# Kernel optimization log

Measured on AMD Instinct MI355X. Metric: run time of the kernel, lower is better.

Reference implementation:

```python
import jax, jax.numpy as jnp
import numpy as np

VOCAB, D, N, K, L = 6144, 1024, 4, 8, 3
D_FF, N_STREAMS, SINK_ITERS = 3072, 4, 20
ALPHA = 4.0      # surrogate sigmoid sharpness
EK_FLOOR = 0.0
B, S = 4, 128

@jax.custom_vjp
def spike(x):
    return (x >= 0.).astype(x.dtype)

def _spike_fwd(x):
    return (x >= 0.).astype(x.dtype), x

def _spike_bwd(x, g):
    s = jax.nn.sigmoid(ALPHA * x)
    return (g * ALPHA * s * (1. - s),)

spike.defvjp(_spike_fwd, _spike_bwd)

def plif_scan(beta, x, v_th):
    # PLIF recurrence over leading time axis. x: (T,B,C); beta, v_th: (C,).
    # v_t = beta*v + (1-beta)*x_t ; heaviside spike (sigmoid surrogate); soft reset.
    # Returns spike current v_th * spike (matches spike_current_activation).
    def step(v, x_t):
        v = beta * v + (1. - beta) * x_t
        s = spike(v - v_th)
        return v - v_th * s, v_th * s
    v0 = jnp.zeros(x.shape[1:], x.dtype)
    _, cur = jax.lax.scan(step, v0, x)
    return cur

def sinkhorn(logits):
    # doubly-stochastic projection (Birkhoff polytope), fixed iteration count
    M = jnp.exp(logits)
    for _ in range(SINK_ITERS):
        M = M / M.sum(1, keepdims=True)
        M = M / M.sum(0, keepdims=True)
    return M

def rmsnorm(x, w, eps=1e-6):
    return x * w * jax.lax.rsqrt(jnp.mean(x * x, axis=-1, keepdims=True) + eps)

def lateral_inhibition(x, w, eps=1e-6):
    xc = x - x.mean(axis=-1, keepdims=True)
    return w * xc * jax.lax.rsqrt(jnp.mean(xc * xc, axis=-1, keepdims=True) + eps)

LAYER_KEYS = ['H_logits','w_pre','w_post','beta_in1','vth_in1','W_in','beta_h','vth_h','W_out','beta_in2','vth_in2','W_gate','beta_gate','vth_gate','W_up','beta_up','vth_up','W_down','halt_w','halt_b']

def layer_forward(h, p):
    # h: (S, B, n, D) multi-stream residual
    Sq, Bq = h.shape[0], h.shape[1]
    H = sinkhorn(p['H_logits'])                                   # (n,n) doubly stochastic
    h_mix = jnp.einsum('mn,sbnd->sbmd', H, h)                     # mHC stream mixing
    x = jnp.einsum('n,sbnd->sbd', jax.nn.softmax(p['w_pre']), h_mix)
    x_tk = jnp.repeat(x, K, axis=0)                               # (S*K, B, D) K-frame unroll
    s1 = plif_scan(p['beta_in1'], x_tk, p['vth_in1'])             # input_neuron1
    sh = plif_scan(p['beta_h'], s1 @ p['W_in'], p['vth_h'])       # snn_block hidden (N*D)
    y_blk = sh @ p['W_out']                                       # (TK,B,D)
    s2 = plif_scan(p['beta_in2'], x_tk + y_blk, p['vth_in2'])     # input_neuron2
    g = plif_scan(p['beta_gate'], s2 @ p['W_gate'], p['vth_gate'])  # snn_ffn gate
    u = plif_scan(p['beta_up'], s2 @ p['W_up'], p['vth_up'])        # snn_ffn up
    y = y_blk + (g * u) @ p['W_down']                             # (TK,B,D)
    yk = y.reshape(Sq, K, Bq, D)
    # PonderNet halting over the K frames of each token
    lam = jax.nn.sigmoid(jnp.einsum('skbd,d->skb', yk, p['halt_w']) + p['halt_b'])
    keep = jnp.cumprod(1. - lam, axis=1)
    prev = jnp.concatenate([jnp.ones_like(keep[:, :1]), keep[:, :-1]], axis=1)
    pk = lam * prev
    pk = pk.at[:, -1].add(1. - pk.sum(axis=1))                    # remainder to last frame
    y_tok = jnp.einsum('skb,skbd->sbd', pk, yk)
    ek = jnp.einsum('skb,k->sb', pk, jnp.arange(1, K + 1, dtype=y.dtype)).mean()
    efc = jnp.maximum(EK_FLOOR - ek, 0.)
    w_post = jax.nn.softmax(p['w_post'])
    h_out = h_mix + w_post[None, None, :, None] * y_tok[:, :, None, :]
    return h_out, ek, efc

def _forward(token_ids, embed, norm_w, decode_W, decode_b, out_norm_w, beta_out, vth_out, stacked):
    emb = embed[token_ids]                                        # (B,S,D)
    h = jnp.transpose(emb, (1, 0, 2))[:, :, None, :]
    h = jnp.broadcast_to(h, (emb.shape[1], emb.shape[0], N_STREAMS, D))  # (S,B,n,D)
    pcs, efcs = [], []
    for l in range(L):
        p = {k: stacked[k][l] for k in LAYER_KEYS}
        h, pc, efc = layer_forward(h, p)
        pcs.append(pc); efcs.append(efc)
    ponder = sum(pcs) / L
    ekf = sum(efcs) / L
    # decode: collapse streams -> K-frame output neuron -> tied embedding logits
    h_coll = h.mean(axis=2)                                       # (S,B,D)
    h_tk = jnp.repeat(h_coll, K, axis=0)                          # (S*K,B,D)
    h_tk = rmsnorm(h_tk, out_norm_w)
    cur = plif_scan(beta_out, h_tk, vth_out)
    decoded = cur.reshape(h_coll.shape[0], K, h_coll.shape[1], D).mean(axis=1)
    decoded = jnp.transpose(decoded, (1, 0, 2))                   # (B,S,D)
    hh = decoded @ decode_W.T + decode_b
    hh = lateral_inhibition(hh, norm_w)
    logits = hh @ embed.T                                         # tied embedding
    return logits, ponder, ekf

def setup_inputs() -> dict:
    key = jax.random.key(0)
    ks = iter(jax.random.split(key, 48))
    def nrm(shape, std):
        return jax.random.normal(next(ks), shape, jnp.float32) * std
    def beta_init(shape):
        return 0.4 + 0.4 * jax.random.uniform(next(ks), shape, jnp.float32)
    def vth_init(shape):
        return 0.1 + 0.3 * jax.random.uniform(next(ks), shape, jnp.float32)
    inp = dict(
        token_ids=jax.random.randint(next(ks), (B, S), 0, VOCAB),
        embed=nrm((VOCAB, D), 0.02),
        norm_w=jnp.ones((D,), jnp.float32),
        decode_W=nrm((D, D), 1. / np.sqrt(D)),
        decode_b=jnp.zeros((D,), jnp.float32),
        out_norm_w=jnp.ones((D,), jnp.float32),
        beta_out=beta_init((D,)), vth_out=vth_init((D,)),
        H_logits=nrm((L, N_STREAMS, N_STREAMS), 0.1),
        w_pre=nrm((L, N_STREAMS), 0.1),
        w_post=nrm((L, N_STREAMS), 0.1),
        beta_in1=beta_init((L, D)), vth_in1=vth_init((L, D)),
        W_in=nrm((L, D, N * D), 1. / np.sqrt(D)),
        beta_h=beta_init((L, N * D)), vth_h=vth_init((L, N * D)),
        W_out=nrm((L, N * D, D), 1. / np.sqrt(N * D)),
        beta_in2=beta_init((L, D)), vth_in2=vth_init((L, D)),
        W_gate=nrm((L, D, D_FF), 1. / np.sqrt(D)),
        beta_gate=beta_init((L, D_FF)), vth_gate=vth_init((L, D_FF)),
        W_up=nrm((L, D, D_FF), 1. / np.sqrt(D)),
        beta_up=beta_init((L, D_FF)), vth_up=vth_init((L, D_FF)),
        W_down=nrm((L, D_FF, D), 1. / np.sqrt(D_FF)),
        halt_w=nrm((L, D), 0.02),
        halt_b=jnp.full((L,), 1.0, jnp.float32),
    )
    return inp

def reference(token_ids, embed, norm_w, decode_W, decode_b, out_norm_w, beta_out, vth_out, H_logits, w_pre, w_post, beta_in1, vth_in1, W_in, beta_h, vth_h, W_out, beta_in2, vth_in2, W_gate, beta_gate, vth_gate, W_up, beta_up, vth_up, W_down, halt_w, halt_b):
    stacked = dict(H_logits=H_logits, w_pre=w_pre, w_post=w_post, beta_in1=beta_in1, vth_in1=vth_in1, W_in=W_in, beta_h=beta_h, vth_h=vth_h, W_out=W_out, beta_in2=beta_in2, vth_in2=vth_in2, W_gate=W_gate, beta_gate=beta_gate, vth_gate=vth_gate, W_up=W_up, beta_up=beta_up, vth_up=vth_up, W_down=W_down, halt_w=halt_w, halt_b=halt_b)
    return _forward(token_ids, embed, norm_w, decode_W, decode_b, out_norm_w, beta_out, vth_out, stacked)
```

## Files before the change

### kernel.cpp

```cpp
#include <hip/hip_runtime.h>
#include <hip/hip_bf16.h>

#define B 4
#define S 128
#define D 1024
#define NS 4
#define KF 8
#define LNUM 3
#define DFF 3072
#define ND 4096
#define T 1024
#define TB 4096
#define VOCABSZ 6144
#define SINKIT 20

typedef unsigned short u16;
typedef __attribute__((ext_vector_type(8))) short short8;
typedef __attribute__((ext_vector_type(4))) float f32x4;

__device__ __forceinline__ void gload16(const void* g, void* l) {
  __builtin_amdgcn_global_load_lds(
      (const __attribute__((address_space(1))) void*)g,
      (__attribute__((address_space(3))) void*)l, 16, 0, 0);
}

__global__ void sink_kernel(const float* __restrict__ Hl, const float* __restrict__ wpre,
                            const float* __restrict__ wpost, float* __restrict__ prm) {
  if (threadIdx.x != 0 || blockIdx.x != 0) return;
  float M[16];
  for (int i = 0; i < 16; ++i) M[i] = expf(Hl[i]);
  for (int it = 0; it < SINKIT; ++it) {
    for (int m = 0; m < 4; ++m) {
      float s = M[m*4+0] + M[m*4+1] + M[m*4+2] + M[m*4+3];
      for (int n = 0; n < 4; ++n) M[m*4+n] /= s;
    }
    for (int n = 0; n < 4; ++n) {
      float s = M[0*4+n] + M[1*4+n] + M[2*4+n] + M[3*4+n];
      for (int m = 0; m < 4; ++m) M[m*4+n] /= s;
    }
  }
  for (int i = 0; i < 16; ++i) prm[i] = M[i];
  float a[4], mx, sm;
  mx = fmaxf(fmaxf(wpre[0], wpre[1]), fmaxf(wpre[2], wpre[3]));
  sm = 0.f; for (int i = 0; i < 4; ++i) { a[i] = expf(wpre[i] - mx); sm += a[i]; }
  for (int i = 0; i < 4; ++i) prm[16+i] = a[i] / sm;
  mx = fmaxf(fmaxf(wpost[0], wpost[1]), fmaxf(wpost[2], wpost[3]));
  sm = 0.f; for (int i = 0; i < 4; ++i) { a[i] = expf(wpost[i] - mx); sm += a[i]; }
  for (int i = 0; i < 4; ++i) prm[20+i] = a[i] / sm;
}

__global__ __launch_bounds__(256)
void gather_kernel(const int* __restrict__ tok, const float* __restrict__ embed,
                   float* __restrict__ h) {
  const int idx = blockIdx.x * 256 + threadIdx.x;
  const int d   = idx % D;
  const int sbn = idx / D;
  const int sb  = sbn / NS;
  const int b   = sb % B, s = sb / B;
  h[idx] = embed[(size_t)tok[b*S + s] * D + d];
}

__global__ __launch_bounds__(256)
void mix_kernel(const float* __restrict__ h, const float* __restrict__ P,
                float* __restrict__ h_mix, float* __restrict__ x) {
  const int idx = blockIdx.x * 256 + threadIdx.x;
  const int d = idx % D, sb = idx / D;
  const float* hp = h + (size_t)sb * NS * D + d;
  const float h0 = hp[0], h1 = hp[D], h2 = hp[2*D], h3 = hp[3*D];
  float xv = 0.f;
  #pragma unroll
  for (int m = 0; m < 4; ++m) {
    float hm = P[m*4+0]*h0 + P[m*4+1]*h1 + P[m*4+2]*h2 + P[m*4+3]*h3;
    h_mix[(size_t)sb * NS * D + m*D + d] = hm;
    xv = fmaf(P[16+m], hm, xv);
  }
  x[idx] = xv;
}

template<bool R1, bool A2>
__global__ __launch_bounds__(256)
void plif_kernel(const float* __restrict__ z1, const float* __restrict__ z2,
                 const float* __restrict__ beta, const float* __restrict__ vth,
                 u16* __restrict__ outp, int C) {
  const int idx = blockIdx.x * 256 + threadIdx.x;
  const int c = idx % C;
  const int stride = B * C;
  const float be = beta[c], vt = vth[c], omb = 1.f - be;
  float v = 0.f;
  constexpr int PF = 32;
  float xA[PF], yA[PF], xB[PF], yB[PF];

#define PLOAD(xa, ya, tb) do {                                               \
    if (R1) {                                                                \
      _Pragma("unroll")                                                      \
      for (int i = 0; i < PF/8; ++i)                                         \
        xa[i] = z1[(size_t)((tb)/8 + i) * stride + idx];                     \
    } else {                                                                 \
      _Pragma("unroll")                                                      \
      for (int i = 0; i < PF; ++i)                                           \
        xa[i] = z1[(size_t)((tb) + i) * stride + idx];                       \
    }                                                                        \
    if (A2) {                                                                \
      _Pragma("unroll")                                                      \
      for (int i = 0; i < PF; ++i)                                           \
        ya[i] = z2[(size_t)((tb) + i) * stride + idx];                       \
    }                                                                        \
  } while (0)

#define PCOMP(xa, ya, tb) do {                                               \
    _Pragma("unroll")                                                        \
    for (int i = 0; i < PF; ++i) {                                           \
      float xt = R1 ? xa[i >> 3] : xa[i];                                    \
      if (A2) xt += ya[i];                                                   \
      v = fmaf(be, v, omb * xt);                                             \
      const bool sp = (v >= vt);                                             \
      if (sp) v -= vt;                                                       \
      outp[(size_t)((tb) + i) * stride + idx] = sp ? (u16)0x3F80 : (u16)0;   \
    }                                                                        \
  } while (0)

  PLOAD(xA, yA, 0);
  for (int tb = 0; tb < T; tb += 2*PF) {
    PLOAD(xB, yB, tb + PF);
    PCOMP(xA, yA, tb);
    if (tb + 2*PF < T) PLOAD(xA, yA, tb + 2*PF);
    PCOMP(xB, yB, tb + PF);
  }
#undef PLOAD
#undef PCOMP
}

__global__ __launch_bounds__(256)
void plif_gu_kernel(const float* __restrict__ z12,
                    const float* __restrict__ bg, const float* __restrict__ vg_,
                    const float* __restrict__ bu, const float* __restrict__ vu_,
                    u16* __restrict__ outp) {
  const int idx = blockIdx.x * 256 + threadIdx.x;
  const int c = idx % DFF, b = idx / DFF;
  const float beg = bg[c], vtg = vg_[c], beu = bu[c], vtu = vu_[c];
  const float og = 1.f - beg, ou = 1.f - beu;
  float vg = 0.f, vu = 0.f;
  constexpr int PF = 32;
  float gA[PF], uA[PF], gB[PF], uB[PF];

#define GLOAD_(ga, ua, tb) do {                                              \
    _Pragma("unroll")                                                        \
    for (int i = 0; i < PF; ++i) {                                           \
      const size_t off_ = ((size_t)((tb) + i) * B + b) * (2*DFF) + c;        \
      ga[i] = z12[off_];                                                     \
      ua[i] = z12[off_ + DFF];                                               \
    }                                                                        \
  } while (0)

#define GCOMP_(ga, ua, tb) do {                                              \
    _Pragma("unroll")                                                        \
    for (int i = 0; i < PF; ++i) {                                           \
      vg = fmaf(beg, vg, og * ga[i]);                                        \
      vu = fmaf(beu, vu, ou * ua[i]);                                        \
      const bool sg = (vg >= vtg), su = (vu >= vtu);                         \
      if (sg) vg -= vtg;                                                     \
      if (su) vu -= vtu;                                                     \
      outp[(size_t)((tb) + i) * (B*DFF) + idx] = (sg && su) ? (u16)0x3F80 : (u16)0; \
    }                                                                        \
  } while (0)

  GLOAD_(gA, uA, 0);
  for (int tb = 0; tb < T; tb += 2*PF) {
    GLOAD_(gB, uB, tb + PF);
    GCOMP_(gA, uA, tb);
    if (tb + 2*PF < T) GLOAD_(gA, uA, tb + 2*PF);
    GCOMP_(gB, uB, tb + PF);
  }
#undef GLOAD_
#undef GCOMP_
}

__global__ __launch_bounds__(256)
void prep_t_kernel(const float* __restrict__ W, const float* __restrict__ sA,
                   const float* __restrict__ sB, float mult,
                   u16* __restrict__ wt, int Kd, int Nd) {
  __shared__ float tile[64][65];
  const int tid = threadIdx.x;
  const int bn = blockIdx.x, bk = blockIdx.y;
  const int c = tid & 63, r0 = (tid >> 6) * 16;
  #pragma unroll
  for (int i = 0; i < 16; ++i) {
    const int r = r0 + i;
    const int kg = bk*64 + r;
    float s = mult;
    if (sA) s *= sA[kg];
    if (sB) s *= sB[kg];
    tile[r][c] = W[(size_t)kg * Nd + bn*64 + c] * s;
  }
  __syncthreads();
  const int K2 = 2 * Kd;
  #pragma unroll
  for (int i = 0; i < 16; ++i) {
    const int nl = r0 + i;
    const float v = tile[c][nl];
    const __hip_bfloat16 h = __float2bfloat16(v);
    const size_t off = (size_t)(bn*64 + nl) * K2 + bk*64 + c;
    wt[off] = *(const u16*)&h;
    const __hip_bfloat16 lo = __float2bfloat16(v - __bfloat162float(h));
    wt[off + Kd] = *(const u16*)&lo;
  }
}

__global__ __launch_bounds__(256)
void prep_nt_kernel(const float* __restrict__ W, const float* __restrict__ sK, float mult,
                    u16* __restrict__ wt, int Kd) {
  const size_t idx = (size_t)blockIdx.x * 256 + threadIdx.x;
  const int k = (int)(idx % Kd);
  const size_t n = idx / Kd;
  const float v = W[idx] * mult * (sK ? sK[k] : 1.f);
  const __hip_bfloat16 h = __float2bfloat16(v);
  const size_t off = n * (2*Kd) + k;
  wt[off] = *(const u16*)&h;
  const __hip_bfloat16 lo = __float2bfloat16(v - __bfloat162float(h));
  wt[off + Kd] = *(const u16*)&lo;
}


template<bool ADDC>
__global__ __launch_bounds__(256)
void mgemm2_kernel(const u16* __restrict__ A, const u16* __restrict__ Bm,
                   const float* __restrict__ Cin, float* __restrict__ Cout,
                   int M, int N, int Astride, int AW, int BW, int Bstride, int K2) {
  __shared__ __align__(16) char lds[49152];
  const int tid = threadIdx.x;
  const int lane = tid & 63, wv = tid >> 6;
  const int wm = wv >> 1, wn = wv & 1;
  const int lr = lane & 15, ks = lane >> 4;
  const int rs3 = (lr >> 1) & 3;

  const int gx = gridDim.x;
  const int nwg = gx * gridDim.y;
  int flat = blockIdx.y * gx + blockIdx.x;
  flat = (flat & 7) * (nwg >> 3) + (flat >> 3);
  const int bn = flat % gx, bm = flat / gx;

  f32x4 acc[4][4];
  #pragma unroll
  for (int i = 0; i < 4; ++i)
    #pragma unroll
    for (int j = 0; j < 4; ++j) acc[i][j] = (f32x4){0.f, 0.f, 0.f, 0.f};

  const size_t am0 = (size_t)bm * 128, bn0 = (size_t)bn * 128;

#define STAGE(bufbase, k0) do {                                                  \
    const int aoff_ = ((k0) >= AW) ? (k0) - AW : (k0);                           \
    const int boff_ = ((k0) >= BW) ? (k0) - BW : (k0);                           \
    _Pragma("unroll")                                                            \
    for (int c_ = 0; c_ < 2; ++c_) {                                             \
      const int bo_ = c_*4096 + wv*1024 + lane*16;                               \
      const int row_ = bo_ >> 6;                                                 \
      const int csrc_ = ((bo_ >> 4) & 3) ^ ((row_ >> 1) & 3);                    \
      gload16((const char*)A + ((am0 + row_) * (size_t)Astride + aoff_ + csrc_*8) * 2, \
              lds + (bufbase) + c_*4096 + wv*1024);                              \
      gload16((const char*)Bm + ((bn0 + row_) * (size_t)Bstride + boff_ + csrc_*8) * 2, \
              lds + (bufbase) + 8192 + c_*4096 + wv*1024);                       \
    }                                                                            \
  } while (0)

  const int nt = K2 >> 5;
  STAGE(0, 0);
  if (nt > 1) STAGE(16384, 32);
  int bc = 0;
  for (int t = 0; t < nt; ++t) {
    if (t + 2 < nt) {
      int bs = bc + 2; if (bs >= 3) bs -= 3;
      STAGE(bs * 16384, (t + 2) << 5);
      asm volatile("s_waitcnt vmcnt(8)\n\ts_barrier" ::: "memory");
    } else if (t + 1 < nt) {
      asm volatile("s_waitcnt vmcnt(4)\n\ts_barrier" ::: "memory");
    } else {
      asm volatile("s_waitcnt vmcnt(0)\n\ts_barrier" ::: "memory");
    }
    const char* la = lds + bc * 16384;
    const char* lb = la + 8192;
    short8 af[4], bf[4];
    #pragma unroll
    for (int f = 0; f < 4; ++f) {
      af[f] = *(const short8*)(la + (wm*64 + f*16 + lr)*64 + ((ks ^ rs3) * 16));
      bf[f] = *(const short8*)(lb + (wn*64 + f*16 + lr)*64 + ((ks ^ rs3) * 16));
    }
    #pragma unroll
    for (int i = 0; i < 4; ++i)
      #pragma unroll
      for (int j = 0; j < 4; ++j)
        acc[i][j] = __builtin_amdgcn_mfma_f32_16x16x32_bf16(af[i], bf[j], acc[i][j], 0, 0, 0);
    asm volatile("s_barrier" ::: "memory");
    bc = bc + 1; if (bc >= 3) bc = 0;
  }
#undef STAGE

  const int col0 = bn*128 + wn*64 + lr;
  #pragma unroll
  for (int i = 0; i < 4; ++i)
    #pragma unroll
    for (int j = 0; j < 4; ++j) {
      const size_t rbase = (size_t)(bm*128 + wm*64 + i*16 + ks*4);
      #pragma unroll
      for (int r = 0; r < 4; ++r) {
        const size_t idx = (rbase + r) * (size_t)N + col0 + j*16;
        float v = acc[i][j][r];
        if (ADDC) v += Cin[idx];
        Cout[idx] = v;
      }
    }
}

__global__ __launch_bounds__(512)
void mgemm3_kernel(const u16* __restrict__ A, const u16* __restrict__ Bm,
                   float* __restrict__ Cout, int M, int N, int Astride, int AW, int K2) {
  __shared__ __align__(16) char lds[98304];
  const int tid = threadIdx.x;
  const int lane = tid & 63, wv = tid >> 6;
  const int wm = wv >> 2, wn = wv & 3;
  const int lr = lane & 15, ks = lane >> 4;
  const int rs3 = (lr >> 1) & 3;

  const int gx = gridDim.x;
  const int nwg = gx * gridDim.y;
  int flat = blockIdx.y * gx + blockIdx.x;
  flat = (flat & 7) * (nwg >> 3) + (flat >> 3);
  const int bn = flat % gx, bm = flat / gx;

  f32x4 acc[8][4];
  #pragma unroll
  for (int i = 0; i < 8; ++i)
    #pragma unroll
    for (int j = 0; j < 4; ++j) acc[i][j] = (f32x4){0.f, 0.f, 0.f, 0.f};

  const size_t am0 = (size_t)bm * 256, bn0 = (size_t)bn * 256;

#define STG(base, k0) do {                                                        \
    const int aoff_ = ((k0) >= AW) ? (k0) - AW : (k0);                            \
    _Pragma("unroll")                                                             \
    for (int c_ = 0; c_ < 2; ++c_) {                                              \
      const int fl_ = c_*8192 + wv*1024 + lane*16;                                \
      const int row_ = fl_ >> 6;                                                  \
      const int csrc_ = ((fl_ >> 4) & 3) ^ ((row_ >> 1) & 3);                     \
      gload16((const char*)A + ((am0 + row_) * (size_t)Astride + aoff_ + csrc_*8) * 2, \
              lds + (base) + c_*8192 + wv*1024);                                  \
      gload16((const char*)Bm + ((bn0 + row_) * (size_t)K2 + (k0) + csrc_*8) * 2, \
              lds + (base) + 16384 + c_*8192 + wv*1024);                          \
    }                                                                             \
  } while (0)

  const int nt = K2 >> 5;
  STG(0, 0);
  if (nt > 1) STG(32768, 32);
  int bc = 0;
  for (int t = 0; t < nt; ++t) {
    if (t + 2 < nt) {
      int bs = bc + 2; if (bs >= 3) bs -= 3;
      STG(bs * 32768, (t + 2) << 5);
      asm volatile("s_waitcnt vmcnt(8)\n\ts_barrier" ::: "memory");
    } else if (t + 1 < nt) {
      asm volatile("s_waitcnt vmcnt(4)\n\ts_barrier" ::: "memory");
    } else {
      asm volatile("s_waitcnt vmcnt(0)\n\ts_barrier" ::: "memory");
    }
    const char* la = lds + bc * 32768;
    const char* lb = la + 16384;
    short8 af[8], bf[4];
    #pragma unroll
    for (int i = 0; i < 8; ++i)
      af[i] = *(const short8*)(la + (wm*128 + i*16 + lr)*64 + ((ks ^ rs3) * 16));
    #pragma unroll
    for (int j = 0; j < 4; ++j)
      bf[j] = *(const short8*)(lb + (wn*64 + j*16 + lr)*64 + ((ks ^ rs3) * 16));
    __builtin_amdgcn_s_setprio(1);
    #pragma unroll
    for (int i = 0; i < 8; ++i)
      #pragma unroll
      for (int j = 0; j < 4; ++j)
        acc[i][j] = __builtin_amdgcn_mfma_f32_16x16x32_bf16(af[i], bf[j], acc[i][j], 0, 0, 0);
    __builtin_amdgcn_s_setprio(0);
    asm volatile("s_barrier" ::: "memory");
    bc = bc + 1; if (bc >= 3) bc = 0;
  }
#undef STG

  const int col0 = bn*256 + wn*64 + lr;
  #pragma unroll
  for (int i = 0; i < 8; ++i)
    #pragma unroll
    for (int j = 0; j < 4; ++j) {
      const size_t rbase = (size_t)(bm*256 + wm*128 + i*16 + ks*4);
      #pragma unroll
      for (int r = 0; r < 4; ++r)
        Cout[(rbase + r) * (size_t)N + col0 + j*16] = acc[i][j][r];
    }
}

__global__ __launch_bounds__(256)
void halt_kernel(const float* __restrict__ y, const float* __restrict__ h_mix,
                 const float* __restrict__ P, const float* __restrict__ hw,
                 const float* __restrict__ hb, float* __restrict__ h_out,
                 float* __restrict__ ek_acc) {
  const int sb = blockIdx.x;
  const int b = sb % B, s = sb / B;
  const int tid = threadIdx.x;
  __shared__ float red[256];
  __shared__ float lam_s[KF];
  __shared__ float pk_s[KF];

  for (int k = 0; k < KF; ++k) {
    const float* yr = y + ((size_t)(s*KF + k) * B + b) * D;
    float p = 0.f;
    for (int d = tid; d < D; d += 256) p = fmaf(yr[d], hw[d], p);
    red[tid] = p; __syncthreads();
    for (int off = 128; off > 0; off >>= 1) {
      if (tid < off) red[tid] += red[tid + off];
      __syncthreads();
    }
    if (tid == 0) lam_s[k] = 1.f / (1.f + expf(-(red[0] + hb[0])));
    __syncthreads();
  }
  if (tid == 0) {
    float keep = 1.f, sum = 0.f, pk[KF];
    #pragma unroll
    for (int k = 0; k < KF; ++k) { pk[k] = lam_s[k] * keep; keep *= (1.f - lam_s[k]); sum += pk[k]; }
    pk[KF-1] += 1.f - sum;
    float ek = 0.f;
    #pragma unroll
    for (int k = 0; k < KF; ++k) { ek += pk[k] * (float)(k + 1); pk_s[k] = pk[k]; }
    atomicAdd(ek_acc, ek);
  }
  __syncthreads();
  for (int d = tid; d < D; d += 256) {
    float yt = 0.f;
    #pragma unroll
    for (int k = 0; k < KF; ++k)
      yt = fmaf(pk_s[k], y[((size_t)(s*KF + k) * B + b) * D + d], yt);
    #pragma unroll
    for (int n = 0; n < NS; ++n) {
      const size_t off = ((size_t)sb * NS + n) * D + d;
      h_out[off] = h_mix[off] + P[20+n] * yt;
    }
  }
}

__global__ __launch_bounds__(256)
void collnorm_kernel(const float* __restrict__ h, const float* __restrict__ w,
                     float* __restrict__ xn) {
  const int sb = blockIdx.x, tid = threadIdx.x;
  __shared__ float red[256];
  float vals[4]; float ss = 0.f;
  #pragma unroll
  for (int i = 0; i < 4; ++i) {
    const int d = tid + i*256;
    const float* hp = h + (size_t)sb * NS * D + d;
    float m = 0.25f * (hp[0] + hp[D] + hp[2*D] + hp[3*D]);
    vals[i] = m; ss += m*m;
  }
  red[tid] = ss; __syncthreads();
  for (int off = 128; off > 0; off >>= 1) { if (tid < off) red[tid] += red[tid + off]; __syncthreads(); }
  const float inv = 1.f / sqrtf(red[0] * (1.f/(float)D) + 1e-6f);
  #pragma unroll
  for (int i = 0; i < 4; ++i) {
    const int d = tid + i*256;
    xn[(size_t)sb * D + d] = vals[i] * w[d] * inv;
  }
}

__global__ __launch_bounds__(256)
void dplif_kernel(const float* __restrict__ xn, const float* __restrict__ beta,
                  const float* __restrict__ vth, u16* __restrict__ dec) {
  const int idx = blockIdx.x * 256 + threadIdx.x;
  const int b = idx / D, d = idx % D;
  const float be = beta[d], vt = vth[d], omb = 1.f - be;
  float v = 0.f;
  for (int s = 0; s < S; ++s) {
    const float xv = xn[((size_t)s * B + b) * D + d];
    float cnt = 0.f;
    #pragma unroll
    for (int k = 0; k < KF; ++k) {
      v = fmaf(be, v, omb * xv);
      if (v >= vt) { v -= vt; cnt += 1.f; }
    }
    const __hip_bfloat16 hb_ = __float2bfloat16(cnt);
    dec[((size_t)b * S + s) * D + d] = *(const u16*)&hb_;
  }
}

__global__ __launch_bounds__(256)
void li_kernel(float* __restrict__ hh, const float* __restrict__ bias,
               const float* __restrict__ w) {
  const int r = blockIdx.x, tid = threadIdx.x;
  __shared__ float red[256];
  float* row = hh + (size_t)r * D;
  float v[4]; float sm = 0.f;
  #pragma unroll
  for (int i = 0; i < 4; ++i) { const int d = tid + i*256; v[i] = row[d] + bias[d]; sm += v[i]; }
  red[tid] = sm; __syncthreads();
  for (int off = 128; off > 0; off >>= 1) { if (tid < off) red[tid] += red[tid + off]; __syncthreads(); }
  const float mean = red[0] * (1.f/(float)D);
  __syncthreads();
  float ss = 0.f;
  #pragma unroll
  for (int i = 0; i < 4; ++i) { v[i] -= mean; ss += v[i]*v[i]; }
  red[tid] = ss; __syncthreads();
  for (int off = 128; off > 0; off >>= 1) { if (tid < off) red[tid] += red[tid + off]; __syncthreads(); }
  const float inv = 1.f / sqrtf(red[0] * (1.f/(float)D) + 1e-6f);
  #pragma unroll
  for (int i = 0; i < 4; ++i) { const int d = tid + i*256; row[d] = w[d] * v[i] * inv; }
}

__global__ __launch_bounds__(256)
void split_kernel(const float* __restrict__ X, u16* __restrict__ xs, int Kd) {
  const size_t idx = (size_t)blockIdx.x * 256 + threadIdx.x;
  const int k = (int)(idx % Kd);
  const size_t n = idx / Kd;
  const float v = X[idx];
  const __hip_bfloat16 h = __float2bfloat16(v);
  const size_t off = n * (2*Kd) + k;
  xs[off] = *(const u16*)&h;
  const __hip_bfloat16 lo = __float2bfloat16(v - __bfloat162float(h));
  xs[off + Kd] = *(const u16*)&lo;
}

__global__ void finalize_kernel(const float* __restrict__ ek_acc, float* __restrict__ tail) {
  if (threadIdx.x != 0 || blockIdx.x != 0) return;
  float ponder = 0.f, ekf = 0.f;
  for (int l = 0; l < LNUM; ++l) {
    float ek = ek_acc[l] * (1.f/(float)(S*B));
    ponder += ek;
    ekf += fmaxf(0.f - ek, 0.f);
  }
  tail[0] = ponder * (1.f/(float)LNUM);
  tail[1] = ekf * (1.f/(float)LNUM);
}

extern "C" void kernel_launch(void* const* d_in, const int* in_sizes, int n_in,
                              void* d_out, int out_size, void* d_ws, size_t ws_size,
                              hipStream_t stream) {
  const int*   tok       = (const int*)  d_in[0];
  const float* embed     = (const float*)d_in[1];
  const float* norm_w    = (const float*)d_in[2];
  const float* decode_W  = (const float*)d_in[3];
  const float* decode_b  = (const float*)d_in[4];
  const float* out_norm  = (const float*)d_in[5];
  const float* beta_out  = (const float*)d_in[6];
  const float* vth_out   = (const float*)d_in[7];
  const float* H_logits  = (const float*)d_in[8];
  const float* w_pre     = (const float*)d_in[9];
  const float* w_post    = (const float*)d_in[10];
  const float* beta_in1  = (const float*)d_in[11];
  const float* vth_in1   = (const float*)d_in[12];
  const float* W_in      = (const float*)d_in[13];
  const float* beta_h    = (const float*)d_in[14];
  const float* vth_h     = (const float*)d_in[15];
  const float* W_out     = (const float*)d_in[16];
  const float* beta_in2  = (const float*)d_in[17];
  const float* vth_in2   = (const float*)d_in[18];
  const float* W_gate    = (const float*)d_in[19];
  const float* beta_gate = (const float*)d_in[20];
  const float* vth_gate  = (const float*)d_in[21];
  const float* W_up      = (const float*)d_in[22];
  const float* beta_up   = (const float*)d_in[23];
  const float* vth_up    = (const float*)d_in[24];
  const float* W_down    = (const float*)d_in[25];
  const float* halt_w    = (const float*)d_in[26];
  const float* halt_b    = (const float*)d_in[27];
  float* out = (float*)d_out;

  float* ws = (float*)d_ws;
  size_t o = 0;
  float* prm   = ws + o; o += 256;
  float* h_cur = ws + o; o += (size_t)S*B*NS*D;
  float* h_mix = ws + o; o += (size_t)S*B*NS*D;
  float* xbuf  = ws + o; o += (size_t)S*B*D;
  float* y_blk = ws + o; o += (size_t)TB*D;
  float* zbig  = ws + o; o += (size_t)TB*2*DFF;
  u16*   spb   = (u16*)(ws + o); o += (size_t)TB*ND/2;
  u16*   s1b   = (u16*)(ws + o); o += (size_t)TB*D/2;
  u16*   s2b   = (u16*)(ws + o); o += (size_t)TB*D/2;
  float* xn    = ws + o; o += (size_t)S*B*D;
  u16*   decb  = (u16*)(ws + o); o += (size_t)B*S*D/2;
  float* hh    = ws + o; o += (size_t)B*S*D;
  u16*   wt    = (u16*)(ws + o); o += (size_t)(2*DFF)*D;
  if (ws_size < o * sizeof(float)) return;

  float* ek_acc = prm + 96;
  hipMemsetAsync(ek_acc, 0, 3 * sizeof(float), stream);

  gather_kernel<<<(S*B*NS*D)/256, 256, 0, stream>>>(tok, embed, h_cur);

  for (int l = 0; l < LNUM; ++l) {
    float* P = prm + l*32;
    sink_kernel<<<1, 64, 0, stream>>>(H_logits + l*16, w_pre + l*4, w_post + l*4, P);
    mix_kernel<<<(S*B*D)/256, 256, 0, stream>>>(h_cur, P, h_mix, xbuf);
    plif_kernel<true,false><<<(B*D)/256, 256, 0, stream>>>(
        xbuf, nullptr, beta_in1 + l*D, vth_in1 + l*D, s1b, D);

    { dim3 gp(ND/64, D/64);
      prep_t_kernel<<<gp, 256, 0, stream>>>(W_in + (size_t)l*D*ND, vth_in1 + l*D, nullptr, 1.f,
                                            wt, D, ND); }
    { dim3 g(ND/256, TB/256);
      mgemm3_kernel<<<g, 512, 0, stream>>>(s1b, wt, zbig, TB, ND, D, D, 2*D); }
    plif_kernel<false,false><<<(B*ND)/256, 256, 0, stream>>>(
        zbig, nullptr, beta_h + l*ND, vth_h + l*ND, spb, ND);

    { dim3 gp(D/64, ND/64);
      prep_t_kernel<<<gp, 256, 0, stream>>>(W_out + (size_t)l*ND*D, vth_h + l*ND, nullptr, 1.f,
                                            wt, ND, D); }
    { dim3 g(D/128, TB/128);
      mgemm2_kernel<false><<<g, 256, 0, stream>>>(spb, wt, nullptr, y_blk, TB, D,
                                                  ND, ND, 2*ND, 2*ND, 2*ND); }
    plif_kernel<true,true><<<(B*D)/256, 256, 0, stream>>>(
        xbuf, y_blk, beta_in2 + l*D, vth_in2 + l*D, s2b, D);

    { dim3 gp(DFF/64, D/64);
      prep_t_kernel<<<gp, 256, 0, stream>>>(W_gate + (size_t)l*D*DFF, vth_in2 + l*D, nullptr, 1.f,
                                            wt, D, DFF);
      prep_t_kernel<<<gp, 256, 0, stream>>>(W_up + (size_t)l*D*DFF, vth_in2 + l*D, nullptr, 1.f,
                                            wt + (size_t)DFF*2*D, D, DFF); }
    { dim3 g((2*DFF)/256, TB/256);
      mgemm3_kernel<<<g, 512, 0, stream>>>(s2b, wt, zbig, TB, 2*DFF, D, D, 2*D); }
    plif_gu_kernel<<<(B*DFF)/256, 256, 0, stream>>>(
        zbig, beta_gate + l*DFF, vth_gate + l*DFF, beta_up + l*DFF, vth_up + l*DFF, spb);

    { dim3 gp(D/64, DFF/64);
      prep_t_kernel<<<gp, 256, 0, stream>>>(W_down + (size_t)l*DFF*D, vth_gate + l*DFF,
                                            vth_up + l*DFF, 1.f, wt, DFF, D); }
    { dim3 g(D/128, TB/128);
      mgemm2_kernel<true><<<g, 256, 0, stream>>>(spb, wt, y_blk, y_blk, TB, D,
                                                 DFF, DFF, 2*DFF, 2*DFF, 2*DFF); }
    halt_kernel<<<S*B, 256, 0, stream>>>(y_blk, h_mix, P, halt_w + l*D, halt_b + l, h_cur, ek_acc + l);
  }

  collnorm_kernel<<<S*B, 256, 0, stream>>>(h_cur, out_norm, xn);
  dplif_kernel<<<(B*D)/256, 256, 0, stream>>>(xn, beta_out, vth_out, decb);

  prep_nt_kernel<<<(D*D)/256, 256, 0, stream>>>(decode_W, vth_out, 0.125f, wt, D);
  { dim3 g(D/128, (B*S)/128);
    mgemm2_kernel<false><<<g, 256, 0, stream>>>(decb, wt, nullptr, hh, B*S, D,
                                                D, D, 2*D, 2*D, 2*D); }
  li_kernel<<<B*S, 256, 0, stream>>>(hh, decode_b, norm_w);

  u16* hh_c  = (u16*)(zbig + 6600000);
  u16* emb_c = (u16*)zbig;
  split_kernel<<<(B*S*D)/256, 256, 0, stream>>>(hh, hh_c, D);
  prep_nt_kernel<<<(VOCABSZ*D)/256, 256, 0, stream>>>(embed, nullptr, 1.f, emb_c, D);
  { dim3 g(VOCABSZ/128, (B*S)/128);
    mgemm2_kernel<false><<<g, 256, 0, stream>>>(hh_c, emb_c, nullptr, out, B*S, VOCABSZ,
                                                2*D, D, 2*D, 2*D, 3*D); }
  finalize_kernel<<<1, 1, 0, stream>>>(ek_acc, out + (out_size - 2));
}
```

Baseline: 2.124 ms.

## Restructure 256x256 GEMM into 8-phase ping-pong pipeline with half-tile staging

Rewrites the mgemm3 main loop from a 3-stage, 32-wide K pipeline into a double-buffered, 64-wide K schedule. Each iteration is split into eight phases that each compute a quadrant of the output tile. Every phase interleaves the LDS fragment reads, the issue of one half-tile global-to-LDS load, and the MFMA block, with explicit vmcnt waits and barriers. The goal is finer-grained overlap of memory traffic with MFMA work, in the style of the hipBLASLt/HipKittens 8-wave ping-pong. In exchange it raises LDS use to 128KB, adds more barriers, and assumes K2 is a multiple of 128.

```diff
diff --git a/kernel.cpp b/kernel.cpp
--- a/kernel.cpp
+++ b/kernel.cpp
@@ -313,7 +313,7 @@
 __global__ __launch_bounds__(512)
 void mgemm3_kernel(const u16* __restrict__ A, const u16* __restrict__ Bm,
                    float* __restrict__ Cout, int M, int N, int Astride, int AW, int K2) {
-  __shared__ __align__(16) char lds[98304];
+  __shared__ __align__(16) char lds[131072];
   const int tid = threadIdx.x;
   const int lane = tid & 63, wv = tid >> 6;
   const int wm = wv >> 2, wn = wv & 3;
@@ -326,72 +326,107 @@
   flat = (flat & 7) * (nwg >> 3) + (flat >> 3);
   const int bn = flat % gx, bm = flat / gx;
 
-  f32x4 acc[8][4];
-  #pragma unroll
-  for (int i = 0; i < 8; ++i)
-    #pragma unroll
-    for (int j = 0; j < 4; ++j) acc[i][j] = (f32x4){0.f, 0.f, 0.f, 0.f};
+  f32x4 acc[2][2][4][2];
+  #pragma unroll
+  for (int a0 = 0; a0 < 2; ++a0)
+    #pragma unroll
+    for (int a1 = 0; a1 < 2; ++a1)
+      #pragma unroll
+      for (int a2 = 0; a2 < 4; ++a2)
+        #pragma unroll
+        for (int a3 = 0; a3 < 2; ++a3)
+          acc[a0][a1][a2][a3] = (f32x4){0.f, 0.f, 0.f, 0.f};
 
   const size_t am0 = (size_t)bm * 256, bn0 = (size_t)bn * 256;
-
-#define STG(base, k0) do {                                                        \
-    const int aoff_ = ((k0) >= AW) ? (k0) - AW : (k0);                            \
+  short8 af[2][4];
+  short8 bf[2][2][2];
+
+#define STG_U(ISB, TILE, HALF) do {                                               \
+    const int tk_ = (TILE) * 64;                                                  \
+    const int aof_ = (ISB) ? tk_ : ((tk_ >= AW) ? tk_ - AW : tk_);                \
     _Pragma("unroll")                                                             \
-    for (int c_ = 0; c_ < 2; ++c_) {                                              \
-      const int fl_ = c_*8192 + wv*1024 + lane*16;                                \
-      const int row_ = fl_ >> 6;                                                  \
+    for (int kk_ = 0; kk_ < 2; ++kk_) {                                           \
+      const int fl_ = wv*1024 + lane*16;                                          \
+      const int row_ = (HALF)*128 + (fl_ >> 6);                                   \
       const int csrc_ = ((fl_ >> 4) & 3) ^ ((row_ >> 1) & 3);                     \
-      gload16((const char*)A + ((am0 + row_) * (size_t)Astride + aoff_ + csrc_*8) * 2, \
-              lds + (base) + c_*8192 + wv*1024);                                  \
-      gload16((const char*)Bm + ((bn0 + row_) * (size_t)K2 + (k0) + csrc_*8) * 2, \
-              lds + (base) + 16384 + c_*8192 + wv*1024);                          \
+      const u16* gp_ = (ISB)                                                      \
+        ? (Bm + (bn0 + row_) * (size_t)K2 + tk_ + kk_*32 + csrc_*8)               \
+        : (A  + (am0 + row_) * (size_t)Astride + aof_ + kk_*32 + csrc_*8);        \
+      gload16(gp_, lds + ((ISB)?65536:0) + ((TILE)&1)*32768 + kk_*16384 + fl_ + (HALF)*8192); \
     }                                                                             \
   } while (0)
 
-  const int nt = K2 >> 5;
-  STG(0, 0);
-  if (nt > 1) STG(32768, 32);
-  int bc = 0;
-  for (int t = 0; t < nt; ++t) {
-    if (t + 2 < nt) {
-      int bs = bc + 2; if (bs >= 3) bs -= 3;
-      STG(bs * 32768, (t + 2) << 5);
-      asm volatile("s_waitcnt vmcnt(8)\n\ts_barrier" ::: "memory");
-    } else if (t + 1 < nt) {
-      asm volatile("s_waitcnt vmcnt(4)\n\ts_barrier" ::: "memory");
-    } else {
-      asm volatile("s_waitcnt vmcnt(0)\n\ts_barrier" ::: "memory");
-    }
-    const char* la = lds + bc * 32768;
-    const char* lb = la + 16384;
-    short8 af[8], bf[4];
-    #pragma unroll
-    for (int i = 0; i < 8; ++i)
-      af[i] = *(const short8*)(la + (wm*128 + i*16 + lr)*64 + ((ks ^ rs3) * 16));
-    #pragma unroll
-    for (int j = 0; j < 4; ++j)
-      bf[j] = *(const short8*)(lb + (wn*64 + j*16 + lr)*64 + ((ks ^ rs3) * 16));
-    __builtin_amdgcn_s_setprio(1);
-    #pragma unroll
-    for (int i = 0; i < 8; ++i)
+#define PHASE(D_, IH, JH, RA, RB, SISB, STILE, SHALF, SVALID) do {                \
+    if (lastit) asm volatile("s_waitcnt vmcnt(0)" ::: "memory");                  \
+    else        asm volatile("s_waitcnt vmcnt(6)" ::: "memory");                  \
+    if (RA) {                                                                     \
+      _Pragma("unroll")                                                           \
+      for (int kk = 0; kk < 2; ++kk)                                              \
+        _Pragma("unroll")                                                         \
+        for (int i = 0; i < 4; ++i)                                               \
+          af[kk][i] = *(const short8*)(lds + (D_)*32768 + kk*16384 +              \
+              ((IH)*128 + wm*64 + i*16 + lr)*64 + ((ks ^ rs3)*16));               \
+    }                                                                             \
+    if (RB) {                                                                     \
+      _Pragma("unroll")                                                           \
+      for (int kk = 0; kk < 2; ++kk)                                              \
+        _Pragma("unroll")                                                         \
+        for (int j = 0; j < 2; ++j)                                               \
+          bf[JH][kk][j] = *(const short8*)(lds + 65536 + (D_)*32768 + kk*16384 +  \
+              ((JH)*128 + wn*32 + j*16 + lr)*64 + ((ks ^ rs3)*16));               \
+    }                                                                             \
+    if (SVALID) STG_U(SISB, STILE, SHALF);                                        \
+    asm volatile("s_barrier" ::: "memory");                                       \
+    asm volatile("s_waitcnt lgkmcnt(0)" ::: "memory");                            \
+    __builtin_amdgcn_sched_barrier(0);                                            \
+    __builtin_amdgcn_s_setprio(1);                                                \
+    _Pragma("unroll")                                                             \
+    for (int i = 0; i < 4; ++i)                                                   \
+      _Pragma("unroll")                                                           \
+      for (int j = 0; j < 2; ++j)                                                 \
+        _Pragma("unroll")                                                         \
+        for (int kk = 0; kk < 2; ++kk)                                            \
+          acc[IH][JH][i][j] = __builtin_amdgcn_mfma_f32_16x16x32_bf16(            \
+              af[kk][i], bf[JH][kk][j], acc[IH][JH][i][j], 0, 0, 0);              \
+    __builtin_amdgcn_s_setprio(0);                                                \
+    asm volatile("s_barrier" ::: "memory");                                       \
+  } while (0)
+
+  const int nt2 = K2 >> 6;
+  const int niter = nt2 >> 1;
+  STG_U(0, 0, 0); STG_U(1, 0, 0); STG_U(0, 0, 1); STG_U(1, 0, 1);
+  STG_U(0, 1, 0); STG_U(1, 1, 0);
+
+  for (int t = 0; t < niter; ++t) {
+    const int t1 = 2*t + 1, t2 = 2*t + 2, t3 = 2*t + 3;
+    const bool s2 = (t2 < nt2), s3 = (t3 < nt2);
+    const bool lastit = (t + 1 >= niter);
+    PHASE(0, 0, 0, 1, 1, 0, t1, 1, true);
+    PHASE(0, 0, 1, 0, 1, 1, t1, 1, true);
+    PHASE(0, 1, 0, 1, 0, 0, t2, 0, s2);
+    PHASE(0, 1, 1, 0, 0, 1, t2, 0, s2);
+    PHASE(1, 0, 0, 1, 1, 0, t2, 1, s2);
+    PHASE(1, 0, 1, 0, 1, 1, t2, 1, s2);
+    PHASE(1, 1, 0, 1, 0, 0, t3, 0, s3);
+    PHASE(1, 1, 1, 0, 0, 1, t3, 0, s3);
+  }
+#undef PHASE
+#undef STG_U
+
+  #pragma unroll
+  for (int ih = 0; ih < 2; ++ih)
+    #pragma unroll
+    for (int jh = 0; jh < 2; ++jh) {
+      const int col0 = bn*256 + jh*128 + wn*32 + lr;
       #pragma unroll
-      for (int j = 0; j < 4; ++j)
-        acc[i][j] = __builtin_amdgcn_mfma_f32_16x16x32_bf16(af[i], bf[j], acc[i][j], 0, 0, 0);
-    __builtin_amdgcn_s_setprio(0);
-    asm volatile("s_barrier" ::: "memory");
-    bc = bc + 1; if (bc >= 3) bc = 0;
-  }
-#undef STG
-
-  const int col0 = bn*256 + wn*64 + lr;
-  #pragma unroll
-  for (int i = 0; i < 8; ++i)
-    #pragma unroll
-    for (int j = 0; j < 4; ++j) {
-      const size_t rbase = (size_t)(bm*256 + wm*128 + i*16 + ks*4);
-      #pragma unroll
-      for (int r = 0; r < 4; ++r)
-        Cout[(rbase + r) * (size_t)N + col0 + j*16] = acc[i][j][r];
+      for (int i = 0; i < 4; ++i)
+        #pragma unroll
+        for (int j = 0; j < 2; ++j) {
+          const size_t rbase = (size_t)(bm*256 + ih*128 + wm*64 + i*16 + ks*4);
+          #pragma unroll
+          for (int r = 0; r < 4; ++r)
+            Cout[(rbase + r) * (size_t)N + col0 + j*16] = acc[ih][jh][i][j][r];
+        }
     }
 }
 
```

Result: faster. 2.071 ms (-2.5%).
